# Kernel tuning notes

Measured on AMD Instinct MI355X. Metric: run time of the kernel, lower is better.

## Reference

```python
import jax, jax.numpy as jnp
import numpy as np

PAD = 32
NCLS = 33  # background + 32 instances
EPS = 1e-6


def lovasz_hinge_flat(logits, labels):
    # logits, labels: flat [P]; labels in {0,1} float
    signs = 2.0 * labels - 1.0
    errors = 1.0 - logits * signs
    perm = jnp.argsort(-errors)  # descending
    errors_sorted = errors[perm]
    gt_sorted = labels[perm]
    gts = gt_sorted.sum()
    intersection = gts - jnp.cumsum(gt_sorted)
    union = gts + jnp.cumsum(1.0 - gt_sorted)
    jaccard = 1.0 - intersection / union
    grad = jnp.concatenate([jaccard[:1], jaccard[1:] - jaccard[:-1]])
    return jnp.dot(jax.nn.relu(errors_sorted), jax.lax.stop_gradient(grad))


def setup_inputs() -> dict:
    key = jax.random.key(0)
    k1, k2, k3, k4, k5, k6 = jax.random.split(key, 6)
    B, C, H, W = 2, 16, 192, 192
    return {
        "y_embeddings": jax.random.normal(k1, (B, C, H, W), dtype=jnp.float32),
        "y_true": jax.random.randint(k2, (B, H, W), 0, NCLS),
        "W1": jax.random.normal(k3, (C, 32), dtype=jnp.float32) * 0.25,
        "b1": jax.random.normal(k4, (32,), dtype=jnp.float32) * 0.1,
        "W2": jax.random.normal(k5, (32,), dtype=jnp.float32) * 0.25,
        "b2": jax.random.normal(k6, (1,), dtype=jnp.float32) * 0.1,
    }


def reference(y_embeddings, y_true, W1, b1, W2, b2):
    def per_image(emb, gt):
        # emb: [C,H,W]; gt: [H,W] int
        emb = jnp.pad(emb, ((0, 0), (PAD, PAD), (PAD, PAD)))
        gt = jnp.pad(gt, ((PAD, PAD), (PAD, PAD)))
        # one-hot instance masks (drop background class 0): [N,Hp,Wp]
        oh = jnp.moveaxis(jax.nn.one_hot(gt, NCLS, dtype=emb.dtype), -1, 0)[1:]
        counts = jax.lax.stop_gradient(oh.sum(axis=(1, 2)) + EPS)  # [N]
        centers = jax.lax.stop_gradient(
            jnp.einsum('nhw,chw->nc', oh, emb) / counts[:, None])  # [N,C]
        # broadcast offsets: [N,C,Hp,Wp]
        sims = (centers[:, :, None, None] - emb[None]) / 32.0
        sims = jnp.clip(sims, -2.0, 2.0)
        feats = jnp.moveaxis(sims, 1, -1)  # [N,Hp,Wp,C]
        h = jax.nn.relu(feats @ W1 + b1)  # [N,Hp,Wp,32]
        logits = h @ W2 + b2[0]  # [N,Hp,Wp]
        return lovasz_hinge_flat(logits.reshape(-1), oh.reshape(-1))

    losses = jax.vmap(per_image)(y_embeddings, y_true)
    return jnp.mean(losses)
```

## Files before the change

### kernel.cpp

```cpp
#include <hip/hip_runtime.h>

#define NBINS 2048
#define IMG_HW 36864
#define T 512
#define BLKPI 72
#define NINST 32
#define CCH 16
#define NH 32
#define PADW 28672
#define NB 2
#define EPSF 1e-6f
#define NACC (NINST * (CCH + 1))

typedef unsigned long long u64;
typedef long long i64;
typedef float f32x4 __attribute__((ext_vector_type(4)));

#define OFF_WG   0
#define OFF_CSUM 32768
#define OFF_MAXB 41472
#define OFF_META 42048

__global__ void __launch_bounds__(256)
k_zero(u64* __restrict__ csum, float* __restrict__ out) {
    int tid = threadIdx.x;
    for (int i = tid; i < NB * NACC; i += 256) csum[i] = 0ull;
    if (tid == 0) out[0] = 0.f;
}

__global__ void __launch_bounds__(T)
k_centers(const float* __restrict__ emb, const int* __restrict__ gt,
          u64* __restrict__ csum, float* __restrict__ maxblk,
          u64* __restrict__ wg) {
    int blk = blockIdx.x, b = blockIdx.y;
    int tid = threadIdx.x;
    __shared__ i64 acc[NACC];
    __shared__ float mred[8];
    for (int i = tid; i < NACC; i += T) acc[i] = 0;
    int gid = (b * BLKPI + blk) * T + tid;
    if (gid < NB * NBINS) wg[gid] = 0ull;
    __syncthreads();

    int pix = blk * T + tid;
    int gtv = gt[(size_t)b * IMG_HW + pix];
    const float* e = emb + (size_t)b * CCH * IMG_HW + pix;
    float ev[CCH];
    float me = 0.f;
#pragma unroll
    for (int c = 0; c < CCH; c++) {
        ev[c] = e[c * IMG_HW];
        me = fmaxf(me, fabsf(ev[c]));
    }
    if (gtv > 0) {
        int n = gtv - 1;
#pragma unroll
        for (int c = 0; c < CCH; c++) {
            i64 fx = (i64)((double)ev[c] * 4294967296.0);
            atomicAdd((u64*)&acc[n * CCH + c], (u64)fx);
        }
        atomicAdd((u64*)&acc[NINST * CCH + n], 1ull);
    }
#pragma unroll
    for (int off = 32; off > 0; off >>= 1) me = fmaxf(me, __shfl_down(me, off, 64));
    if ((tid & 63) == 0) mred[tid >> 6] = me;
    __syncthreads();
    if (tid == 0) {
        float m = 0.f;
        for (int w = 0; w < T / 64; w++) m = fmaxf(m, mred[w]);
        maxblk[b * BLKPI + blk] = m;
    }
    u64* cb = csum + (size_t)b * NACC;
    for (int i = tid; i < NACC; i += T) {
        u64 v = (u64)acc[i];
        if (v) atomicAdd(&cb[i], v);
    }
}

__global__ void __launch_bounds__(T, 2)
k_hist(const float* __restrict__ emb, const int* __restrict__ gt,
       const float* __restrict__ W1, const float* __restrict__ b1,
       const float* __restrict__ W2, const float* __restrict__ b2,
       const u64* __restrict__ csum, const float* __restrict__ maxblk,
       float* __restrict__ meta, u64* __restrict__ wg) {
    __shared__ unsigned int hist[NBINS];
    __shared__ __align__(16) float q_s[NINST][NH];
    __shared__ float a_s[NINST][CCH];
    __shared__ float redf[8], redm[8];
    __shared__ float semax[NINST];
    __shared__ float scons[1];

    int pixblk = blockIdx.x, b = blockIdx.y;
    int tid = threadIdx.x;

    int pix = pixblk * T + tid;
    int gtv = gt[(size_t)b * IMG_HW + pix];
    const float* e = emb + (size_t)b * CCH * IMG_HW + pix;
    float u[CCH];
#pragma unroll
    for (int c = 0; c < CCH; c++) u[c] = e[c * IMG_HW];

    for (int i = tid; i < NBINS; i += T) hist[i] = 0u;

    const u64* cb = csum + (size_t)b * NACC;
    float a_own;
    {
        int n = tid >> 4;
        float cnt = (float)(i64)cb[NINST * CCH + n] + EPSF;
        float a = (float)((double)(i64)cb[tid] * (1.0 / 4294967296.0)) / cnt * (1.f / 32.f);
        a_s[n][tid & 15] = a;
        a_own = fabsf(a);
    }
    float me = (tid < BLKPI) ? maxblk[b * BLKPI + tid] : 0.f;
#pragma unroll
    for (int off = 32; off > 0; off >>= 1) {
        me = fmaxf(me, __shfl_down(me, off, 64));
        a_own = fmaxf(a_own, __shfl_down(a_own, off, 64));
    }
    if ((tid & 63) == 0) { redf[tid >> 6] = me; redm[tid >> 6] = a_own; }
    __syncthreads();

    float maxug = 0.f, maxa = 0.f;
#pragma unroll
    for (int w = 0; w < T / 64; w++) {
        maxug = fmaxf(maxug, redf[w]);
        maxa = fmaxf(maxa, redm[w]);
    }
    maxug *= (1.f / 32.f);
    float b2v = b2[0];

    {
        int n = tid >> 4, jg = tid & 15;
        float lo_sum = 0.f, hi_sum = 0.f;
#pragma unroll
        for (int jj = 0; jj < 2; jj++) {
            int j = jg * 2 + jj;
            float s = b1[j], smin = s, smax = s;
#pragma unroll
            for (int c = 0; c < CCH; c++) {
                float w = W1[c * NH + j];
                float a = a_s[n][c];
                float lo = fmaxf(a - maxug, -2.f);
                float hi = fminf(a + maxug, 2.f);
                s += a * w;
                if (w >= 0.f) { smin += lo * w; smax += hi * w; }
                else          { smin += hi * w; smax += lo * w; }
            }
            q_s[n][j] = s;
            float hlo = fmaxf(smin, 0.f), hhi = fmaxf(smax, 0.f);
            float w2 = W2[j];
            if (w2 >= 0.f) { lo_sum += hlo * w2; hi_sum += hhi * w2; }
            else           { lo_sum += hhi * w2; hi_sum += hlo * w2; }
        }
#pragma unroll
        for (int off = 8; off > 0; off >>= 1) {
            lo_sum += __shfl_down(lo_sum, off, 16);
            hi_sum += __shfl_down(hi_sum, off, 16);
        }
        if ((tid & 15) == 0)
            semax[n] = 1.f + fmaxf(b2v + hi_sum, -(b2v + lo_sum));
    }
    __syncthreads();
    if (tid < 32) {
        float mval = semax[tid];
#pragma unroll
        for (int off = 16; off > 0; off >>= 1) mval = fmaxf(mval, __shfl_down(mval, off, 32));
        if (tid == 0) {
            float sc = (float)NBINS / (mval + 1e-3f);
            scons[0] = sc;
            if (pixblk == 0) meta[b] = sc;
        }
    }
    if (pixblk == 0 && tid >= 64 && tid < 96) {
        float g = (float)(i64)cb[NINST * CCH + (tid - 64)];
#pragma unroll
        for (int off = 16; off > 0; off >>= 1) g += __shfl_down(g, off, 32);
        if (tid == 64) meta[4 + b] = g;
    }
    __syncthreads();
    float scale = scons[0];

    if (pixblk == 0 && tid < NINST) {
        int n = tid;
        float logit = b2v;
        for (int j = 0; j < NH; j++) {
            float s = b1[j];
#pragma unroll
            for (int c = 0; c < CCH; c++)
                s += fminf(fmaxf(a_s[n][c], -2.f), 2.f) * W1[c * NH + j];
            logit += fmaxf(s, 0.f) * W2[j];
        }
        float er = 1.f + logit;
        if (er > 0.f) {
            int bin = min((int)(er * scale), NBINS - 1);
            atomicAdd(&wg[(size_t)b * NBINS + bin], (u64)PADW);
        }
    }

    float maxu = 0.f;
#pragma unroll
    for (int c = 0; c < CCH; c++) {
        u[c] *= (1.f / 32.f);
        maxu = fmaxf(maxu, fabsf(u[c]));
    }

    if (maxu + maxa <= 2.f) {
        const f32x4 z4 = {0.f, 0.f, 0.f, 0.f};
        f32x4 v4[8];
#pragma unroll
        for (int jj = 0; jj < 8; jj++) v4[jj] = z4;
#pragma unroll
        for (int c = 0; c < CCH; c++) {
            const f32x4* w1r = reinterpret_cast<const f32x4*>(W1 + c * NH);
            float uc = u[c];
#pragma unroll
            for (int jj = 0; jj < 8; jj++) v4[jj] += uc * w1r[jj];
        }
        f32x4 w2v[8];
        {
            const f32x4* w2p = reinterpret_cast<const f32x4*>(W2);
#pragma unroll
            for (int jj = 0; jj < 8; jj++) w2v[jj] = w2p[jj];
        }
#pragma unroll 2
        for (int n = 0; n < NINST; n++) {
            const f32x4* qn = reinterpret_cast<const f32x4*>(&q_s[n][0]);
            f32x4 acc = z4;
#pragma unroll
            for (int jj = 0; jj < 8; jj++) {
                f32x4 t = qn[jj] - v4[jj];
                t[0] = fmaxf(t[0], 0.f);
                t[1] = fmaxf(t[1], 0.f);
                t[2] = fmaxf(t[2], 0.f);
                t[3] = fmaxf(t[3], 0.f);
                acc += t * w2v[jj];
            }
            float logit = b2v + ((acc[0] + acc[1]) + (acc[2] + acc[3]));
            unsigned int label = (gtv == n + 1) ? 1u : 0u;
            float er = label ? (1.f - logit) : (1.f + logit);
            if (er > 0.f) {
                int bin = min((int)(er * scale), NBINS - 1);
                atomicAdd(&hist[bin], 1u | (label << 16));
            }
        }
    } else {
        for (int n = 0; n < NINST; n++) {
            float logit = b2v;
            for (int j = 0; j < NH; j++) {
                float s = b1[j];
#pragma unroll
                for (int c = 0; c < CCH; c++) {
                    float f = fminf(fmaxf(a_s[n][c] - u[c], -2.f), 2.f);
                    s += f * W1[c * NH + j];
                }
                logit += fmaxf(s, 0.f) * W2[j];
            }
            unsigned int label = (gtv == n + 1) ? 1u : 0u;
            float er = label ? (1.f - logit) : (1.f + logit);
            if (er > 0.f) {
                int bin = min((int)(er * scale), NBINS - 1);
                atomicAdd(&hist[bin], 1u | (label << 16));
            }
        }
    }
    __syncthreads();
    {
        u64* wgb = wg + (size_t)b * NBINS;
        for (int i = tid; i < NBINS; i += T) {
            unsigned int h = hist[i];
            if (h) atomicAdd(&wgb[i], (u64)(h & 0xffffu) | ((u64)(h >> 16) << 32));
        }
    }
}

__global__ void __launch_bounds__(1024)
k_loss(const u64* __restrict__ wg, const float* __restrict__ meta,
       float* __restrict__ out) {
    int b = blockIdx.x;
    int tid = threadIdx.x;
    const u64* wgb = wg + (size_t)b * NBINS;
    double G = (double)meta[4 + b];
    double invscale = 1.0 / (double)meta[b];
    const int BPT = NBINS / 1024;

    u64 tot = 0;
#pragma unroll
    for (int k = 0; k < BPT; k++) {
        int bin = NBINS - 1 - (tid * BPT + k);
        tot += wgb[bin];
    }
    u64 incl = tot;
    int lane = tid & 63, wid = tid >> 6;
#pragma unroll
    for (int off = 1; off < 64; off <<= 1) {
        u64 x = __shfl_up(incl, off, 64);
        if (lane >= off) incl += x;
    }
    __shared__ u64 wpart[16];
    __shared__ double dred[16];
    if (lane == 63) wpart[wid] = incl;
    __syncthreads();
    u64 woff = 0;
    for (int w = 0; w < wid; w++) woff += wpart[w];
    u64 excl = woff + incl - tot;
    unsigned int p = (unsigned int)(excl & 0xffffffffull);
    unsigned int cs = (unsigned int)(excl >> 32);

    double loss = 0.0;
    if (G > 0.5) {
#pragma unroll
        for (int k = 0; k < BPT; k++) {
            int bin = NBINS - 1 - (tid * BPT + k);
            u64 v = wgb[bin];
            unsigned int w = (unsigned int)(v & 0xffffffffull);
            unsigned int g = (unsigned int)(v >> 32);
            if (w) {
                double Js = 1.0 - (G - (double)cs) / (G + (double)p - (double)cs);
                unsigned int pe = p + w, ce = cs + g;
                double Je = 1.0 - (G - (double)ce) / (G + (double)pe - (double)ce);
                double rep = ((double)bin + 0.5) * invscale;
                loss += rep * (Je - Js);
                p = pe;
                cs = ce;
            }
        }
    }
#pragma unroll
    for (int off = 32; off > 0; off >>= 1) loss += __shfl_down(loss, off, 64);
    if (lane == 0) dred[wid] = loss;
    __syncthreads();
    if (tid == 0) {
        double t = 0;
        for (int w = 0; w < 16; w++) t += dred[w];
        atomicAdd(out, (float)(t * 0.5));
    }
}

extern "C" void kernel_launch(void* const* d_in, const int* in_sizes, int n_in,
                              void* d_out, int out_size, void* d_ws, size_t ws_size,
                              hipStream_t stream) {
    const float* emb = (const float*)d_in[0];
    const int* gt = (const int*)d_in[1];
    const float* W1 = (const float*)d_in[2];
    const float* b1 = (const float*)d_in[3];
    const float* W2 = (const float*)d_in[4];
    const float* b2 = (const float*)d_in[5];
    float* out = (float*)d_out;
    char* ws = (char*)d_ws;

    u64* wg = (u64*)(ws + OFF_WG);
    u64* csum = (u64*)(ws + OFF_CSUM);
    float* maxblk = (float*)(ws + OFF_MAXB);
    float* meta = (float*)(ws + OFF_META);

    k_zero<<<dim3(1), 256, 0, stream>>>(csum, out);
    k_centers<<<dim3(BLKPI, NB), T, 0, stream>>>(emb, gt, csum, maxblk, wg);
    k_hist<<<dim3(BLKPI, NB), T, 0, stream>>>(emb, gt, W1, b1, W2, b2,
                                              csum, maxblk, meta, wg);
    k_loss<<<dim3(NB), 1024, 0, stream>>>(wg, meta, out);
}
```

Before: 39.96 us.

## Fold zero and loss kernels into neighbours via per-block partials and last-block ticket

Removes the zeroing kernel by having each centers block write its private accumulator partials to global memory instead of atomically adding into a pre-zeroed buffer. The hist kernel then reduces the 72 partials per batch itself. The separate loss kernel is replaced by a last-block-done ticket at the end of the hist kernel, and that last block computes the loss for both batches. This cuts two kernel launches and their gaps, at the cost of every hist block redundantly reducing the partials and the final loss running on one 512-thread block.

```diff
diff --git a/kernel.cpp b/kernel.cpp
--- a/kernel.cpp
+++ b/kernel.cpp
@@ -17,28 +17,23 @@
 typedef float f32x4 __attribute__((ext_vector_type(4)));
 
 #define OFF_WG   0
-#define OFF_CSUM 32768
-#define OFF_MAXB 41472
-#define OFF_META 42048
-
-__global__ void __launch_bounds__(256)
-k_zero(u64* __restrict__ csum, float* __restrict__ out) {
-    int tid = threadIdx.x;
-    for (int i = tid; i < NB * NACC; i += 256) csum[i] = 0ull;
-    if (tid == 0) out[0] = 0.f;
-}
+#define OFF_PART 32768
+#define OFF_MAXB 659456
+#define OFF_META 660032
+#define OFF_TKT  660064
 
 __global__ void __launch_bounds__(T)
 k_centers(const float* __restrict__ emb, const int* __restrict__ gt,
-          u64* __restrict__ csum, float* __restrict__ maxblk,
-          u64* __restrict__ wg) {
+          i64* __restrict__ partials, float* __restrict__ maxblk,
+          u64* __restrict__ wg, unsigned int* __restrict__ ticket) {
     int blk = blockIdx.x, b = blockIdx.y;
     int tid = threadIdx.x;
     __shared__ i64 acc[NACC];
-    __shared__ float mred[8];
+    __shared__ float mred[T / 64];
     for (int i = tid; i < NACC; i += T) acc[i] = 0;
     int gid = (b * BLKPI + blk) * T + tid;
     if (gid < NB * NBINS) wg[gid] = 0ull;
+    if (gid == 0) *ticket = 0u;
     __syncthreads();
 
     int pix = blk * T + tid;
@@ -66,26 +61,26 @@
     __syncthreads();
     if (tid == 0) {
         float m = 0.f;
+#pragma unroll
         for (int w = 0; w < T / 64; w++) m = fmaxf(m, mred[w]);
         maxblk[b * BLKPI + blk] = m;
     }
-    u64* cb = csum + (size_t)b * NACC;
-    for (int i = tid; i < NACC; i += T) {
-        u64 v = (u64)acc[i];
-        if (v) atomicAdd(&cb[i], v);
-    }
+    i64* pb = partials + ((size_t)b * BLKPI + blk) * NACC;
+    for (int i = tid; i < NACC; i += T) pb[i] = acc[i];
 }
 
 __global__ void __launch_bounds__(T, 2)
 k_hist(const float* __restrict__ emb, const int* __restrict__ gt,
        const float* __restrict__ W1, const float* __restrict__ b1,
        const float* __restrict__ W2, const float* __restrict__ b2,
-       const u64* __restrict__ csum, const float* __restrict__ maxblk,
-       float* __restrict__ meta, u64* __restrict__ wg) {
+       const i64* __restrict__ partials, const float* __restrict__ maxblk,
+       float* __restrict__ meta, u64* __restrict__ wg,
+       unsigned int* __restrict__ ticket, float* __restrict__ out) {
     __shared__ unsigned int hist[NBINS];
     __shared__ __align__(16) float q_s[NINST][NH];
     __shared__ float a_s[NINST][CCH];
-    __shared__ float redf[8], redm[8];
+    __shared__ float cnt_s[NINST];
+    __shared__ float redf[T / 64], redm[T / 64];
     __shared__ float semax[NINST];
     __shared__ float scons[1];
 
@@ -101,22 +96,32 @@
 
     for (int i = tid; i < NBINS; i += T) hist[i] = 0u;
 
-    const u64* cb = csum + (size_t)b * NACC;
-    float a_own;
+    const i64* pp = partials + (size_t)b * BLKPI * NACC;
+    i64 chsum = 0;
+#pragma unroll 8
+    for (int s = 0; s < BLKPI; s++) chsum += pp[(size_t)s * NACC + tid];
+    if (tid < NINST) {
+        i64 cs = 0;
+#pragma unroll 8
+        for (int s = 0; s < BLKPI; s++) cs += pp[(size_t)s * NACC + NINST * CCH + tid];
+        cnt_s[tid] = (float)cs;
+    }
+    __syncthreads();
+    int n_own = tid >> 4;
+    float a;
     {
-        int n = tid >> 4;
-        float cnt = (float)(i64)cb[NINST * CCH + n] + EPSF;
-        float a = (float)((double)(i64)cb[tid] * (1.0 / 4294967296.0)) / cnt * (1.f / 32.f);
-        a_s[n][tid & 15] = a;
-        a_own = fabsf(a);
-    }
+        float cnt = cnt_s[n_own] + EPSF;
+        a = (float)((double)chsum * (1.0 / 4294967296.0)) / cnt * (1.f / 32.f);
+        a_s[n_own][tid & 15] = a;
+    }
+    float a_abs = fabsf(a);
     float me = (tid < BLKPI) ? maxblk[b * BLKPI + tid] : 0.f;
 #pragma unroll
     for (int off = 32; off > 0; off >>= 1) {
         me = fmaxf(me, __shfl_down(me, off, 64));
-        a_own = fmaxf(a_own, __shfl_down(a_own, off, 64));
-    }
-    if ((tid & 63) == 0) { redf[tid >> 6] = me; redm[tid >> 6] = a_own; }
+        a_abs = fmaxf(a_abs, __shfl_down(a_abs, off, 64));
+    }
+    if ((tid & 63) == 0) { redf[tid >> 6] = me; redm[tid >> 6] = a_abs; }
     __syncthreads();
 
     float maxug = 0.f, maxa = 0.f;
@@ -138,10 +143,10 @@
 #pragma unroll
             for (int c = 0; c < CCH; c++) {
                 float w = W1[c * NH + j];
-                float a = a_s[n][c];
-                float lo = fmaxf(a - maxug, -2.f);
-                float hi = fminf(a + maxug, 2.f);
-                s += a * w;
+                float av = a_s[n][c];
+                float lo = fmaxf(av - maxug, -2.f);
+                float hi = fminf(av + maxug, 2.f);
+                s += av * w;
                 if (w >= 0.f) { smin += lo * w; smax += hi * w; }
                 else          { smin += hi * w; smax += lo * w; }
             }
@@ -171,7 +176,7 @@
         }
     }
     if (pixblk == 0 && tid >= 64 && tid < 96) {
-        float g = (float)(i64)cb[NINST * CCH + (tid - 64)];
+        float g = cnt_s[tid - 64];
 #pragma unroll
         for (int off = 16; off > 0; off >>= 1) g += __shfl_down(g, off, 32);
         if (tid == 64) meta[4 + b] = g;
@@ -270,69 +275,83 @@
             if (h) atomicAdd(&wgb[i], (u64)(h & 0xffffu) | ((u64)(h >> 16) << 32));
         }
     }
-}
-
-__global__ void __launch_bounds__(1024)
-k_loss(const u64* __restrict__ wg, const float* __restrict__ meta,
-       float* __restrict__ out) {
-    int b = blockIdx.x;
-    int tid = threadIdx.x;
-    const u64* wgb = wg + (size_t)b * NBINS;
-    double G = (double)meta[4 + b];
-    double invscale = 1.0 / (double)meta[b];
-    const int BPT = NBINS / 1024;
-
-    u64 tot = 0;
-#pragma unroll
-    for (int k = 0; k < BPT; k++) {
-        int bin = NBINS - 1 - (tid * BPT + k);
-        tot += wgb[bin];
-    }
-    u64 incl = tot;
+
+    __threadfence();
+    __syncthreads();
+    __shared__ unsigned int stk;
+    if (tid == 0)
+        stk = __hip_atomic_fetch_add(ticket, 1u, __ATOMIC_ACQ_REL,
+                                     __HIP_MEMORY_SCOPE_AGENT);
+    __syncthreads();
+    if (stk != (unsigned)(NB * BLKPI - 1)) return;
+
+    __shared__ u64 wpart[T / 64];
+    __shared__ double dred[T / 64];
+    const int BPT = NBINS / T;
+    double total = 0.0;
     int lane = tid & 63, wid = tid >> 6;
-#pragma unroll
-    for (int off = 1; off < 64; off <<= 1) {
-        u64 x = __shfl_up(incl, off, 64);
-        if (lane >= off) incl += x;
-    }
-    __shared__ u64 wpart[16];
-    __shared__ double dred[16];
-    if (lane == 63) wpart[wid] = incl;
-    __syncthreads();
-    u64 woff = 0;
-    for (int w = 0; w < wid; w++) woff += wpart[w];
-    u64 excl = woff + incl - tot;
-    unsigned int p = (unsigned int)(excl & 0xffffffffull);
-    unsigned int cs = (unsigned int)(excl >> 32);
-
-    double loss = 0.0;
-    if (G > 0.5) {
+    for (int bb = 0; bb < NB; bb++) {
+        const u64* wgs = wg + (size_t)bb * NBINS;
+        unsigned int gu = __hip_atomic_load((unsigned int*)&meta[4 + bb],
+                                            __ATOMIC_RELAXED, __HIP_MEMORY_SCOPE_AGENT);
+        unsigned int su = __hip_atomic_load((unsigned int*)&meta[bb],
+                                            __ATOMIC_RELAXED, __HIP_MEMORY_SCOPE_AGENT);
+        double G = (double)__uint_as_float(gu);
+        double invscale = 1.0 / (double)__uint_as_float(su);
+
+        u64 tot = 0;
 #pragma unroll
         for (int k = 0; k < BPT; k++) {
             int bin = NBINS - 1 - (tid * BPT + k);
-            u64 v = wgb[bin];
-            unsigned int w = (unsigned int)(v & 0xffffffffull);
-            unsigned int g = (unsigned int)(v >> 32);
-            if (w) {
-                double Js = 1.0 - (G - (double)cs) / (G + (double)p - (double)cs);
-                unsigned int pe = p + w, ce = cs + g;
-                double Je = 1.0 - (G - (double)ce) / (G + (double)pe - (double)ce);
-                double rep = ((double)bin + 0.5) * invscale;
-                loss += rep * (Je - Js);
-                p = pe;
-                cs = ce;
-            }
-        }
-    }
-#pragma unroll
-    for (int off = 32; off > 0; off >>= 1) loss += __shfl_down(loss, off, 64);
-    if (lane == 0) dred[wid] = loss;
-    __syncthreads();
-    if (tid == 0) {
-        double t = 0;
-        for (int w = 0; w < 16; w++) t += dred[w];
-        atomicAdd(out, (float)(t * 0.5));
-    }
+            tot += __hip_atomic_load(&wgs[bin], __ATOMIC_RELAXED,
+                                     __HIP_MEMORY_SCOPE_AGENT);
+        }
+        u64 incl = tot;
+#pragma unroll
+        for (int off = 1; off < 64; off <<= 1) {
+            u64 x = __shfl_up(incl, off, 64);
+            if (lane >= off) incl += x;
+        }
+        if (lane == 63) wpart[wid] = incl;
+        __syncthreads();
+        u64 woff = 0;
+        for (int w = 0; w < wid; w++) woff += wpart[w];
+        u64 excl = woff + incl - tot;
+        unsigned int p = (unsigned int)(excl & 0xffffffffull);
+        unsigned int cs = (unsigned int)(excl >> 32);
+
+        double loss = 0.0;
+        if (G > 0.5) {
+#pragma unroll
+            for (int k = 0; k < BPT; k++) {
+                int bin = NBINS - 1 - (tid * BPT + k);
+                u64 v = __hip_atomic_load(&wgs[bin], __ATOMIC_RELAXED,
+                                          __HIP_MEMORY_SCOPE_AGENT);
+                unsigned int w = (unsigned int)(v & 0xffffffffull);
+                unsigned int g = (unsigned int)(v >> 32);
+                if (w) {
+                    double Js = 1.0 - (G - (double)cs) / (G + (double)p - (double)cs);
+                    unsigned int pe = p + w, ce = cs + g;
+                    double Je = 1.0 - (G - (double)ce) / (G + (double)pe - (double)ce);
+                    double rep = ((double)bin + 0.5) * invscale;
+                    loss += rep * (Je - Js);
+                    p = pe;
+                    cs = ce;
+                }
+            }
+        }
+#pragma unroll
+        for (int off = 32; off > 0; off >>= 1) loss += __shfl_down(loss, off, 64);
+        if (lane == 0) dred[wid] = loss;
+        __syncthreads();
+        if (tid == 0) {
+            double t = 0;
+            for (int w = 0; w < T / 64; w++) t += dred[w];
+            total += t;
+        }
+        __syncthreads();
+    }
+    if (tid == 0) out[0] = (float)(total * 0.5);
 }
 
 extern "C" void kernel_launch(void* const* d_in, const int* in_sizes, int n_in,
@@ -348,13 +367,12 @@
     char* ws = (char*)d_ws;
 
     u64* wg = (u64*)(ws + OFF_WG);
-    u64* csum = (u64*)(ws + OFF_CSUM);
+    i64* partials = (i64*)(ws + OFF_PART);
     float* maxblk = (float*)(ws + OFF_MAXB);
     float* meta = (float*)(ws + OFF_META);
-
-    k_zero<<<dim3(1), 256, 0, stream>>>(csum, out);
-    k_centers<<<dim3(BLKPI, NB), T, 0, stream>>>(emb, gt, csum, maxblk, wg);
+    unsigned int* ticket = (unsigned int*)(ws + OFF_TKT);
+
+    k_centers<<<dim3(BLKPI, NB), T, 0, stream>>>(emb, gt, partials, maxblk, wg, ticket);
     k_hist<<<dim3(BLKPI, NB), T, 0, stream>>>(emb, gt, W1, b1, W2, b2,
-                                              csum, maxblk, meta, wg);
-    k_loss<<<dim3(NB), 1024, 0, stream>>>(wg, meta, out);
+                                              partials, maxblk, meta, wg, ticket, out);
 }
```

Measured after the change: 61.95 us. 55.0% more time.
